# Performance work log

Measured on AMD Instinct MI355X. Metric: run time of the kernel, lower is better.

Reference implementation:

```python
import jax, jax.numpy as jnp
import numpy as np

NUM_HEADS = 16
VALUE_SIZE = 64
MODEL_SIZE = 1024
BATCH = 4
SEQ = 1024


def setup_inputs() -> dict:
    key = jax.random.key(0)
    ks = jax.random.split(key, 5)
    scale = 1.0 / np.sqrt(MODEL_SIZE)
    x = jax.random.normal(ks[0], (BATCH, SEQ, MODEL_SIZE), dtype=jnp.float32)
    w_q = jax.random.normal(ks[1], (MODEL_SIZE, NUM_HEADS * VALUE_SIZE), dtype=jnp.float32) * scale
    w_kv = jax.random.normal(ks[2], (MODEL_SIZE, NUM_HEADS * VALUE_SIZE), dtype=jnp.float32) * scale
    w_o = jax.random.normal(ks[3], (NUM_HEADS * VALUE_SIZE, MODEL_SIZE), dtype=jnp.float32) * scale
    # original init is Constant(0.0); use small random values for a non-trivial test
    k_weights = jax.random.normal(ks[4], (1, NUM_HEADS, 1, VALUE_SIZE), dtype=jnp.float32) * 0.02
    return {"x": x, "w_q": w_q, "w_kv": w_kv, "w_o": w_o, "k_weights": k_weights}


def reference(x, w_q, w_kv, w_o, k_weights):
    b, L, d = x.shape
    h, v = NUM_HEADS, VALUE_SIZE
    # projections (no bias); q scaled by 1/sqrt(model_size)
    q = (x @ w_q) * (1.0 / jnp.sqrt(jnp.asarray(d, x.dtype)))
    q = q.reshape(b, L, h, v).transpose(0, 2, 1, 3)    # b h l v
    kv = (x @ w_kv).reshape(b, L, h, v).transpose(0, 2, 1, 3)  # b h l v
    # learned per-head key scaling on the shared k=v tensor
    k = kv * (1.0 + k_weights)
    logits = jnp.einsum('bhik,bhjk->bhij', q, k)       # b h L L
    mask = jnp.tril(jnp.ones((L, L), dtype=bool))
    logits = jnp.where(mask, logits, jnp.asarray(-1e6, logits.dtype))
    a = jax.nn.softmax(logits, axis=-1)
    y = jnp.einsum('bhij,bhjv->bhiv', a, kv)           # attend over shared kv
    y = y.transpose(0, 2, 1, 3).reshape(b, L, h * v)
    return y @ w_o
```

## Files before the change

kernel.cpp:

```cpp
#include <hip/hip_runtime.h>
#include <hip/hip_bf16.h>
#include <stdint.h>

#define BATCH 4
#define SEQ   1024
#define DMODEL 1024
#define NH    16
#define DV    64

typedef short bf8 __attribute__((ext_vector_type(8)));
typedef float f4  __attribute__((ext_vector_type(4)));

static __device__ __forceinline__ short f2bf(float f) {
    union { float f; uint32_t u; } a; a.f = f;
    uint32_t r = a.u + 0x7FFF + ((a.u >> 16) & 1);
    return (short)(r >> 16);
}

static __device__ __forceinline__ f4 mfma16(bf8 a, bf8 b, f4 c) {
    return __builtin_amdgcn_mfma_f32_16x16x32_bf16(a, b, c, 0, 0, 0);
}

static __device__ __forceinline__ void gload16(const short* g, short* l) {
    __builtin_amdgcn_global_load_lds((const __attribute__((address_space(1))) void*)g,
                                     (__attribute__((address_space(3))) void*)l,
                                     16, 0, 0);
}


__global__ void cvt_x_kernel(const float* __restrict__ x, short* __restrict__ xb) {
    int i = blockIdx.x * blockDim.x + threadIdx.x;
    float4 v = ((const float4*)x)[i];
    short4 o;
    o.x = f2bf(v.x); o.y = f2bf(v.y); o.z = f2bf(v.z); o.w = f2bf(v.w);
    ((short4*)xb)[i] = o;
}

__global__ void transpose_w_kernel(const float* __restrict__ wq, const float* __restrict__ wkv,
                                   const float* __restrict__ wo,
                                   short* __restrict__ wqkvt, short* __restrict__ wot) {
    __shared__ float tile[32][33];
    int z = blockIdx.z;
    const float* w = (z == 0) ? wq : (z == 1) ? wkv : wo;
    short* wt = (z == 0) ? wqkvt : (z == 1) ? (wqkvt + (1u << 20)) : wot;
    int bx = blockIdx.x, by = blockIdx.y;
    int tx = threadIdx.x, ty = threadIdx.y;
    #pragma unroll
    for (int i = 0; i < 4; i++)
        tile[ty + i * 8][tx] = w[(size_t)(by * 32 + ty + i * 8) * 1024 + bx * 32 + tx];
    __syncthreads();
    #pragma unroll
    for (int i = 0; i < 4; i++)
        wt[(size_t)(bx * 32 + ty + i * 8) * 1024 + by * 32 + tx] = f2bf(tile[tx][ty + i * 8]);
}


template <int MODE>
__global__ __launch_bounds__(256) void gemm_bt_kernel(
    const short* __restrict__ A, const short* __restrict__ Bt,
    int M, int N, int K,
    const float* __restrict__ kw,
    short* __restrict__ q_out, short* __restrict__ kv_out, short* __restrict__ kvT_out,
    float* __restrict__ c_out)
{
    __shared__ short As[128 * 64];
    __shared__ short Bs[128 * 64];

    int tid = threadIdx.x;
    int wave = tid >> 6, lane = tid & 63;
    int quad = lane >> 4, l16 = lane & 15;
    int m0 = blockIdx.y * 128;
    int n0 = blockIdx.x * 128;
    int wm = (wave >> 1) * 64;
    int wn = (wave & 1) * 64;
    int sw = l16 & 7;

    f4 acc[4][4] = {};

    for (int k0 = 0; k0 < K; k0 += 64) {
        __syncthreads();
        #pragma unroll
        for (int c = 0; c < 4; c++) {
            int flat = c * 256 + tid;
            int row = flat >> 3;
            int seg = (flat & 7) ^ (row & 7);
            gload16(A  + (size_t)(m0 + row) * K + k0 + seg * 8, As + flat * 8);
            gload16(Bt + (size_t)(n0 + row) * K + k0 + seg * 8, Bs + flat * 8);
        }
        __syncthreads();

        #pragma unroll
        for (int kk = 0; kk < 2; kk++) {
            bf8 af[4], bfr[4];
            #pragma unroll
            for (int i = 0; i < 4; i++)
                af[i] = *(const bf8*)(As + (wm + i * 16 + l16) * 64 + ((kk * 4 + quad) ^ sw) * 8);
            #pragma unroll
            for (int j = 0; j < 4; j++)
                bfr[j] = *(const bf8*)(Bs + (wn + j * 16 + l16) * 64 + ((kk * 4 + quad) ^ sw) * 8);
            #pragma unroll
            for (int i = 0; i < 4; i++)
                #pragma unroll
                for (int j = 0; j < 4; j++)
                    acc[i][j] = mfma16(af[i], bfr[j], acc[i][j]);
        }
    }

    #pragma unroll
    for (int i = 0; i < 4; i++) {
        #pragma unroll
        for (int j = 0; j < 4; j++) {
            int n = n0 + wn + j * 16 + l16;
            int mb = m0 + wm + i * 16 + quad * 4;
            float v0 = acc[i][j][0], v1 = acc[i][j][1], v2 = acc[i][j][2], v3 = acc[i][j][3];
            if (MODE == 1) {
                if (n < 1024) {
                    float kws = 0.03125f * (1.0f + kw[n]);
                    q_out[(size_t)(mb + 0) * 1024 + n] = f2bf(v0 * kws);
                    q_out[(size_t)(mb + 1) * 1024 + n] = f2bf(v1 * kws);
                    q_out[(size_t)(mb + 2) * 1024 + n] = f2bf(v2 * kws);
                    q_out[(size_t)(mb + 3) * 1024 + n] = f2bf(v3 * kws);
                } else {
                    int n2 = n - 1024;
                    short s0 = f2bf(v0), s1 = f2bf(v1), s2 = f2bf(v2), s3 = f2bf(v3);
                    kv_out[(size_t)(mb + 0) * 1024 + n2] = s0;
                    kv_out[(size_t)(mb + 1) * 1024 + n2] = s1;
                    kv_out[(size_t)(mb + 2) * 1024 + n2] = s2;
                    kv_out[(size_t)(mb + 3) * 1024 + n2] = s3;
                    int bh = ((mb >> 10) << 4) + (n2 >> 6);
                    short4 tv; tv.x = s0; tv.y = s1; tv.z = s2; tv.w = s3;
                    *(short4*)(kvT_out + (size_t)(bh * 64 + (n2 & 63)) * 1024 + (mb & 1023)) = tv;
                }
            } else {
                c_out[(size_t)(mb + 0) * N + n] = v0;
                c_out[(size_t)(mb + 1) * N + n] = v1;
                c_out[(size_t)(mb + 2) * N + n] = v2;
                c_out[(size_t)(mb + 3) * N + n] = v3;
            }
        }
    }
}


#define PLD 72

__global__ __launch_bounds__(256) void attn_kernel(
    const short* __restrict__ qg, const short* __restrict__ kvg,
    const short* __restrict__ kvTg, short* __restrict__ yg)
{
    int bh = blockIdx.y;
    int b = bh >> 4, h = bh & 15;
    int x = blockIdx.x;
    int tid = threadIdx.x;
    int wave = tid >> 6, lane = tid & 63;
    int quad = lane >> 4, l16 = lane & 15;
    int qa0 = x * 64;
    int qb0 = (15 - x) * 64;
    int ntiles = 16 - x;

    __shared__ short Ks[2][64 * 64];
    __shared__ short Vs[2][64 * 64];
    __shared__ short Ps[4][16 * PLD];
    short* myP = &Ps[wave][0];

    const short* qpa = qg + (size_t)(b * 1024 + qa0 + wave * 16 + l16) * 1024 + h * 64;
    const short* qpb = qg + (size_t)(b * 1024 + qb0 + wave * 16 + l16) * 1024 + h * 64;
    bf8 qa_0 = *(const bf8*)(qpa + quad * 8);
    bf8 qa_1 = *(const bf8*)(qpa + 32 + quad * 8);
    bf8 qb_0 = *(const bf8*)(qpb + quad * 8);
    bf8 qb_1 = *(const bf8*)(qpb + 32 + quad * 8);

    bf8 ones;
    #pragma unroll
    for (int j = 0; j < 8; j++) ones[j] = (short)0x3F80;

    f4 oa[4] = {}, ob[4] = {};
    f4 lsa = {}, lsb = {};
    int rowbaseA = qa0 + wave * 16 + quad * 4;
    int rowbaseB = qb0 + wave * 16 + quad * 4;

    auto stage = [&](int jt) {
        short* dstK = &Ks[jt & 1][0];
        short* dstV = &Vs[jt & 1][0];
        int j0 = jt * 64;
        #pragma unroll
        for (int k = 0; k < 2; k++) {
            int flat = k * 256 + tid;
            int row = flat >> 3;
            int lseg = (flat & 7) ^ (row & 7);
            gload16(kvg + (size_t)(b * 1024 + j0 + row) * 1024 + h * 64 + lseg * 8,
                    dstK + flat * 8);
            gload16(kvTg + (size_t)(bh * 64 + row) * 1024 + j0 + lseg * 8,
                    dstV + flat * 8);
        }
    };

    auto proc = [&](bf8 qf0, bf8 qf1, int rowbase, int j0,
                    const short* K, const short* V, f4 (&o)[4], f4& lsum) {
        f4 s[4];
        #pragma unroll
        for (int c = 0; c < 4; c++) {
            int row = c * 16 + l16;
            int swz = row & 7;
            bf8 kb0 = *(const bf8*)(K + row * 64 + (quad ^ swz) * 8);
            bf8 kb1 = *(const bf8*)(K + row * 64 + (((quad + 4) ^ swz)) * 8);
            f4 t = {};
            t = mfma16(qf0, kb0, t);
            t = mfma16(qf1, kb1, t);
            s[c] = t;
        }
        #pragma unroll
        for (int r = 0; r < 4; r++) {
            int qi = rowbase + r;
            float p0 = (j0 + l16      <= qi) ? __expf(s[0][r]) : 0.0f;
            float p1 = (j0 + 16 + l16 <= qi) ? __expf(s[1][r]) : 0.0f;
            float p2 = (j0 + 32 + l16 <= qi) ? __expf(s[2][r]) : 0.0f;
            float p3 = (j0 + 48 + l16 <= qi) ? __expf(s[3][r]) : 0.0f;
            int prow = quad * 4 + r;
            myP[prow * PLD + l16]      = f2bf(p0);
            myP[prow * PLD + 16 + l16] = f2bf(p1);
            myP[prow * PLD + 32 + l16] = f2bf(p2);
            myP[prow * PLD + 48 + l16] = f2bf(p3);
        }
        bf8 pf0 = *(const bf8*)(myP + l16 * PLD + quad * 8);
        bf8 pf1 = *(const bf8*)(myP + l16 * PLD + 32 + quad * 8);
        lsum = mfma16(pf0, ones, lsum);
        lsum = mfma16(pf1, ones, lsum);
        #pragma unroll
        for (int t = 0; t < 4; t++) {
            int vrow = t * 16 + l16;
            int swz = vrow & 7;
            bf8 vb0 = *(const bf8*)(V + vrow * 64 + (quad ^ swz) * 8);
            bf8 vb1 = *(const bf8*)(V + vrow * 64 + (((quad + 4) ^ swz)) * 8);
            o[t] = mfma16(pf0, vb0, o[t]);
            o[t] = mfma16(pf1, vb1, o[t]);
        }
    };

    stage(0);

    for (int jt = 0; jt < ntiles; jt++) {
        __syncthreads();
        if (jt + 1 < ntiles) stage(jt + 1);
        const short* K = &Ks[jt & 1][0];
        const short* V = &Vs[jt & 1][0];
        int j0 = jt * 64;
        proc(qb_0, qb_1, rowbaseB, j0, K, V, ob, lsb);
        if (jt <= x)
            proc(qa_0, qa_1, rowbaseA, j0, K, V, oa, lsa);
    }

    {
        float r0 = 1.0f / lsa[0], r1 = 1.0f / lsa[1], r2 = 1.0f / lsa[2], r3 = 1.0f / lsa[3];
        #pragma unroll
        for (int t = 0; t < 4; t++) {
            size_t base = (size_t)(b * SEQ + rowbaseA) * (NH * DV) + h * DV + t * 16 + l16;
            yg[base]                 = f2bf(oa[t][0] * r0);
            yg[base + 1 * (NH * DV)] = f2bf(oa[t][1] * r1);
            yg[base + 2 * (NH * DV)] = f2bf(oa[t][2] * r2);
            yg[base + 3 * (NH * DV)] = f2bf(oa[t][3] * r3);
        }
    }
    {
        float r0 = 1.0f / lsb[0], r1 = 1.0f / lsb[1], r2 = 1.0f / lsb[2], r3 = 1.0f / lsb[3];
        #pragma unroll
        for (int t = 0; t < 4; t++) {
            size_t base = (size_t)(b * SEQ + rowbaseB) * (NH * DV) + h * DV + t * 16 + l16;
            yg[base]                 = f2bf(ob[t][0] * r0);
            yg[base + 1 * (NH * DV)] = f2bf(ob[t][1] * r1);
            yg[base + 2 * (NH * DV)] = f2bf(ob[t][2] * r2);
            yg[base + 3 * (NH * DV)] = f2bf(ob[t][3] * r3);
        }
    }
}


extern "C" void kernel_launch(void* const* d_in, const int* in_sizes, int n_in,
                              void* d_out, int out_size, void* d_ws, size_t ws_size,
                              hipStream_t stream) {
    const float* x    = (const float*)d_in[0];
    const float* w_q  = (const float*)d_in[1];
    const float* w_kv = (const float*)d_in[2];
    const float* w_o  = (const float*)d_in[3];
    const float* kw   = (const float*)d_in[4];
    float* out = (float*)d_out;

    char* ws = (char*)d_ws;
    short* xb    = (short*)(ws);
    short* wqkvt = (short*)(ws + ( 8u << 20));
    short* wot   = (short*)(ws + (12u << 20));
    short* qp    = (short*)(ws + (14u << 20));
    short* kvb   = (short*)(ws + (22u << 20));
    short* kvT   = (short*)(ws + (30u << 20));
    short* yb    = (short*)(ws + (38u << 20));

    cvt_x_kernel<<<4096, 256, 0, stream>>>(x, xb);
    transpose_w_kernel<<<dim3(32, 32, 3), dim3(32, 8), 0, stream>>>(w_q, w_kv, w_o, wqkvt, wot);

    gemm_bt_kernel<1><<<dim3(16, 32), 256, 0, stream>>>(
        xb, wqkvt, BATCH * SEQ, 2048, DMODEL,
        kw, qp, kvb, kvT, (float*)nullptr);

    attn_kernel<<<dim3(8, BATCH * NH), 256, 0, stream>>>(qp, kvb, kvT, yb);

    gemm_bt_kernel<2><<<dim3(8, 32), 256, 0, stream>>>(
        yb, wot, BATCH * SEQ, DMODEL, DMODEL,
        nullptr, nullptr, nullptr, nullptr, out);
}
```

Measured before the change: 160.5 us.

## Stage kvT transpose through LDS and shrink output GEMM tile

The projection GEMM now writes its transposed KV output by staging bf16 values in shared memory and issuing coalesced 16-byte row stores, replacing scattered 8-byte strided stores. The output projection gets its own kernel with a 64x128 tile, which doubles the block count to 512 so more of the GPU's compute units are busy. The cost is extra LDS traffic and barriers in the projection epilogue, plus less data reuse per block in the output GEMM.

```diff
diff --git a/kernel.cpp b/kernel.cpp
--- a/kernel.cpp
+++ b/kernel.cpp
@@ -55,16 +55,15 @@
 }
 
 
-template <int MODE>
-__global__ __launch_bounds__(256) void gemm_bt_kernel(
+__global__ __launch_bounds__(256) void gemm_proj_kernel(
     const short* __restrict__ A, const short* __restrict__ Bt,
-    int M, int N, int K,
     const float* __restrict__ kw,
-    short* __restrict__ q_out, short* __restrict__ kv_out, short* __restrict__ kvT_out,
-    float* __restrict__ c_out)
+    short* __restrict__ q_out, short* __restrict__ kv_out, short* __restrict__ kvT_out)
 {
-    __shared__ short As[128 * 64];
-    __shared__ short Bs[128 * 64];
+    __shared__ short SM[2 * 128 * 64];
+    short* As = SM;
+    short* Bs = SM + 128 * 64;
+    const int K = DMODEL;
 
     int tid = threadIdx.x;
     int wave = tid >> 6, lane = tid & 63;
@@ -113,31 +112,116 @@
             int n = n0 + wn + j * 16 + l16;
             int mb = m0 + wm + i * 16 + quad * 4;
             float v0 = acc[i][j][0], v1 = acc[i][j][1], v2 = acc[i][j][2], v3 = acc[i][j][3];
-            if (MODE == 1) {
-                if (n < 1024) {
-                    float kws = 0.03125f * (1.0f + kw[n]);
-                    q_out[(size_t)(mb + 0) * 1024 + n] = f2bf(v0 * kws);
-                    q_out[(size_t)(mb + 1) * 1024 + n] = f2bf(v1 * kws);
-                    q_out[(size_t)(mb + 2) * 1024 + n] = f2bf(v2 * kws);
-                    q_out[(size_t)(mb + 3) * 1024 + n] = f2bf(v3 * kws);
-                } else {
-                    int n2 = n - 1024;
-                    short s0 = f2bf(v0), s1 = f2bf(v1), s2 = f2bf(v2), s3 = f2bf(v3);
-                    kv_out[(size_t)(mb + 0) * 1024 + n2] = s0;
-                    kv_out[(size_t)(mb + 1) * 1024 + n2] = s1;
-                    kv_out[(size_t)(mb + 2) * 1024 + n2] = s2;
-                    kv_out[(size_t)(mb + 3) * 1024 + n2] = s3;
-                    int bh = ((mb >> 10) << 4) + (n2 >> 6);
-                    short4 tv; tv.x = s0; tv.y = s1; tv.z = s2; tv.w = s3;
-                    *(short4*)(kvT_out + (size_t)(bh * 64 + (n2 & 63)) * 1024 + (mb & 1023)) = tv;
+            if (n < 1024) {
+                float kws = 0.03125f * (1.0f + kw[n]);
+                q_out[(size_t)(mb + 0) * 1024 + n] = f2bf(v0 * kws);
+                q_out[(size_t)(mb + 1) * 1024 + n] = f2bf(v1 * kws);
+                q_out[(size_t)(mb + 2) * 1024 + n] = f2bf(v2 * kws);
+                q_out[(size_t)(mb + 3) * 1024 + n] = f2bf(v3 * kws);
+            } else {
+                int n2 = n - 1024;
+                kv_out[(size_t)(mb + 0) * 1024 + n2] = f2bf(v0);
+                kv_out[(size_t)(mb + 1) * 1024 + n2] = f2bf(v1);
+                kv_out[(size_t)(mb + 2) * 1024 + n2] = f2bf(v2);
+                kv_out[(size_t)(mb + 3) * 1024 + n2] = f2bf(v3);
+            }
+        }
+    }
+
+    if (n0 >= 1024) {
+        const int TST = 136;
+        short* T = SM;
+        int n2base = n0 - 1024;
+        int mloc = m0 & 1023;
+        int bq = m0 >> 10;
+        #pragma unroll
+        for (int hn = 0; hn < 2; hn++) {
+            __syncthreads();
+            if ((wave & 1) == hn) {
+                #pragma unroll
+                for (int i = 0; i < 4; i++) {
+                    #pragma unroll
+                    for (int j = 0; j < 4; j++) {
+                        int nl = j * 16 + l16;
+                        int ml = wm + i * 16 + quad * 4;
+                        short4 tv;
+                        tv.x = f2bf(acc[i][j][0]); tv.y = f2bf(acc[i][j][1]);
+                        tv.z = f2bf(acc[i][j][2]); tv.w = f2bf(acc[i][j][3]);
+                        *(short4*)(T + nl * TST + ml) = tv;
+                    }
                 }
-            } else {
-                c_out[(size_t)(mb + 0) * N + n] = v0;
-                c_out[(size_t)(mb + 1) * N + n] = v1;
-                c_out[(size_t)(mb + 2) * N + n] = v2;
-                c_out[(size_t)(mb + 3) * N + n] = v3;
             }
-        }
+            __syncthreads();
+            #pragma unroll
+            for (int c = 0; c < 4; c++) {
+                int flat = c * 256 + tid;
+                int row = flat >> 4;
+                int seg = flat & 15;
+                bf8 vseg = *(const bf8*)(T + row * TST + seg * 8);
+                int n2 = n2base + hn * 64 + row;
+                int bh = (bq << 4) + (n2 >> 6);
+                *(bf8*)(kvT_out + (size_t)(bh * 64 + (n2 & 63)) * 1024 + mloc + seg * 8) = vseg;
+            }
+        }
+    }
+}
+
+
+__global__ __launch_bounds__(256) void gemm_out_kernel(
+    const short* __restrict__ A, const short* __restrict__ Bt,
+    float* __restrict__ c_out)
+{
+    __shared__ short As[64 * 64];
+    __shared__ short Bs[128 * 64];
+    const int K = DMODEL;
+
+    int tid = threadIdx.x;
+    int wave = tid >> 6, lane = tid & 63;
+    int quad = lane >> 4, l16 = lane & 15;
+    int m0 = blockIdx.y * 64;
+    int n0 = blockIdx.x * 128;
+    int wm = wave * 16;
+    int sw = l16 & 7;
+
+    f4 acc[8] = {};
+
+    for (int k0 = 0; k0 < K; k0 += 64) {
+        __syncthreads();
+        #pragma unroll
+        for (int c = 0; c < 2; c++) {
+            int flat = c * 256 + tid;
+            int row = flat >> 3;
+            int seg = (flat & 7) ^ (row & 7);
+            gload16(A + (size_t)(m0 + row) * K + k0 + seg * 8, As + flat * 8);
+        }
+        #pragma unroll
+        for (int c = 0; c < 4; c++) {
+            int flat = c * 256 + tid;
+            int row = flat >> 3;
+            int seg = (flat & 7) ^ (row & 7);
+            gload16(Bt + (size_t)(n0 + row) * K + k0 + seg * 8, Bs + flat * 8);
+        }
+        __syncthreads();
+
+        #pragma unroll
+        for (int kk = 0; kk < 2; kk++) {
+            bf8 af = *(const bf8*)(As + (wm + l16) * 64 + ((kk * 4 + quad) ^ sw) * 8);
+            #pragma unroll
+            for (int j = 0; j < 8; j++) {
+                bf8 bf_ = *(const bf8*)(Bs + (j * 16 + l16) * 64 + ((kk * 4 + quad) ^ sw) * 8);
+                acc[j] = mfma16(af, bf_, acc[j]);
+            }
+        }
+    }
+
+    #pragma unroll
+    for (int j = 0; j < 8; j++) {
+        int n = n0 + j * 16 + l16;
+        int mb = m0 + wm + quad * 4;
+        c_out[(size_t)(mb + 0) * 1024 + n] = acc[j][0];
+        c_out[(size_t)(mb + 1) * 1024 + n] = acc[j][1];
+        c_out[(size_t)(mb + 2) * 1024 + n] = acc[j][2];
+        c_out[(size_t)(mb + 3) * 1024 + n] = acc[j][3];
     }
 }
 
@@ -297,13 +381,10 @@
     cvt_x_kernel<<<4096, 256, 0, stream>>>(x, xb);
     transpose_w_kernel<<<dim3(32, 32, 3), dim3(32, 8), 0, stream>>>(w_q, w_kv, w_o, wqkvt, wot);
 
-    gemm_bt_kernel<1><<<dim3(16, 32), 256, 0, stream>>>(
-        xb, wqkvt, BATCH * SEQ, 2048, DMODEL,
-        kw, qp, kvb, kvT, (float*)nullptr);
+    gemm_proj_kernel<<<dim3(16, 32), 256, 0, stream>>>(
+        xb, wqkvt, kw, qp, kvb, kvT);
 
     attn_kernel<<<dim3(8, BATCH * NH), 256, 0, stream>>>(qp, kvb, kvT, yb);
 
-    gemm_bt_kernel<2><<<dim3(8, 32), 256, 0, stream>>>(
-        yb, wot, BATCH * SEQ, DMODEL, DMODEL,
-        nullptr, nullptr, nullptr, nullptr, out);
-}
+    gemm_out_kernel<<<dim3(8, 64), 256, 0, stream>>>(yb, wot, out);
+}
```

Measured after the change: 159.4 us. About the same (-0.7%).
